# Kernel optimization log

Hardware: AMD Instinct MI355X
Metric: run time of the kernel (lower is better)

Reference implementation:

```python
import jax, jax.numpy as jnp
import numpy as np

N_NODES = 100000
N_EDGES = 1250000
IN_DIM = 128
HID_DIM = 64
OUT_DIM = 16


def setup_inputs() -> dict:
    key = jax.random.key(0)
    k1, k2, k3, k4, k5, k6, k7 = jax.random.split(key, 7)
    x = jax.random.normal(k1, (N_NODES, IN_DIM), dtype=jnp.float32)
    edge_index = jax.random.randint(k2, (2, N_EDGES), 0, N_NODES, dtype=jnp.int64)
    s = 1.0 / np.sqrt(IN_DIM)
    W1 = jax.random.uniform(k3, (IN_DIM, HID_DIM), jnp.float32, -s, s)
    b1 = jax.random.uniform(k4, (HID_DIM,), jnp.float32, -s, s)
    s2 = 1.0 / np.sqrt(HID_DIM)
    W2 = jax.random.uniform(k5, (HID_DIM, OUT_DIM), jnp.float32, -s2, s2)
    b2 = jax.random.uniform(k6, (OUT_DIM,), jnp.float32, -s2, s2)
    return {"x": x, "edge_index": edge_index, "W1": W1, "b1": b1, "W2": W2, "b2": b2}


def reference(x, edge_index, W1, b1, W2, b2):
    # GCNConv (PyG default): linear transform, add self-loops, symmetric norm,
    # gather-scatter aggregation, bias. Then relu -> linear -> log_softmax.
    N = x.shape[0]
    loop = jnp.arange(N, dtype=edge_index.dtype)
    src = jnp.concatenate([edge_index[0], loop])  # message sources
    dst = jnpp_concat = jnp.concatenate([edge_index[1], loop])  # message targets
    # degree (with self-loops) computed on destination nodes
    deg = jax.ops.segment_sum(jnp.ones_like(dst, dtype=x.dtype), dst, num_segments=N)
    deg_inv_sqrt = jnp.where(deg > 0, jax.lax.rsqrt(deg), 0.0)
    norm = deg_inv_sqrt[src] * deg_inv_sqrt[dst]  # [E+N]
    h = x @ W1  # [N, hid] -- transform before aggregation (fewer bytes moved)
    msg = h[src] * norm[:, None]  # gather: [E+N, hid]
    agg = jax.ops.segment_sum(msg, dst, num_segments=N) + b1  # scatter-add
    h = jax.nn.relu(agg)
    logits = h @ W2 + b2
    return jax.nn.log_softmax(logits, axis=-1)
```

## Files before the change

kernel.cpp:

```cpp
#include <hip/hip_runtime.h>

#define N_NODES 100000
#define N_EDGES 1250000
#define IN_DIM  128
#define HID     64
#define OUTD    16
#define ROW     64
#define NRANGE  8
#define RSIZE   12500
#define NCHUNK  128
#define CHUNK   9768
#define FILLB   (NRANGE * NCHUNK)

typedef __attribute__((ext_vector_type(8))) short  short8;
typedef __attribute__((ext_vector_type(4))) float  floatx4;

__device__ __forceinline__ unsigned short f2bf(float f) {
    unsigned u = __float_as_uint(f);
    u += 0x7fffu + ((u >> 16) & 1u);
    return (unsigned short)(u >> 16);
}
__device__ __forceinline__ float bf2f_lo(unsigned u) { return __uint_as_float(u << 16); }
__device__ __forceinline__ float bf2f_hi(unsigned u) { return __uint_as_float(u & 0xffff0000u); }

__global__ __launch_bounds__(256) void zero_cursor(int* __restrict__ cursor,
                                                   unsigned* __restrict__ hb_dummy) {
    int i = blockIdx.x * 256 + threadIdx.x;
    if (i < N_NODES) cursor[i] = 0;
    if (i < 32) hb_dummy[i] = 0u;
}

__global__ __launch_bounds__(256) void fill_kernel(const int* __restrict__ src,
                                                   const int* __restrict__ dst,
                                                   int* __restrict__ cursor,
                                                   int* __restrict__ csr) {
    const int r  = blockIdx.x & 7;
    const int c  = blockIdx.x >> 3;
    const int lo = r * RSIZE;
    const int q1 = min(N_EDGES, (c + 1) * CHUNK) >> 2;
    for (int q = (c * CHUNK >> 2) + threadIdx.x; q < q1; q += 256) {
        int4 d4 = ((const int4*)dst)[q];
        int  e  = q << 2;
#pragma unroll
        for (int u = 0; u < 4; u++) {
            int d = (u == 0) ? d4.x : (u == 1) ? d4.y : (u == 2) ? d4.z : d4.w;
            if ((unsigned)(d - lo) < (unsigned)RSIZE) {
                int s = src[e + u];
                int p = atomicAdd(&cursor[d], 1);
                if (p < ROW) csr[(size_t)d * ROW + p] = s;
            }
        }
    }
}

__global__ __launch_bounds__(256) void gemm_mfma(const float* __restrict__ x,
                                                 const float* __restrict__ W1,
                                                 const int* __restrict__ cursor,
                                                 float* __restrict__ dis,
                                                 unsigned short* __restrict__ hb) {
    __shared__ unsigned short xs[16][132];
    __shared__ unsigned short w1t[64][132];

    const int m0 = blockIdx.x * 16;

    for (int idx = threadIdx.x; idx < 16 * IN_DIM; idx += 256) {
        int m = idx >> 7, k = idx & 127;
        xs[m][k] = f2bf(x[(size_t)(m0 + m) * IN_DIM + k]);
    }
    for (int idx = threadIdx.x; idx < IN_DIM * HID; idx += 256) {
        int k = idx >> 6, n = idx & 63;
        w1t[n][k] = f2bf(W1[idx]);
    }
    __syncthreads();

    const int lane = threadIdx.x & 63;
    const int n0   = (threadIdx.x >> 6) * 16;
    const int mrow = lane & 15;
    const int quad = lane >> 4;

    floatx4 acc = {0.f, 0.f, 0.f, 0.f};
#pragma unroll
    for (int k0 = 0; k0 < IN_DIM; k0 += 32) {
        short8 a = *(const short8*)&xs[mrow][k0 + quad * 8];
        short8 b = *(const short8*)&w1t[n0 + mrow][k0 + quad * 8];
        acc = __builtin_amdgcn_mfma_f32_16x16x32_bf16(a, b, acc, 0, 0, 0);
    }

#pragma unroll
    for (int reg = 0; reg < 4; reg++) {
        int m = quad * 4 + reg;
        float di = rsqrtf((float)cursor[m0 + m] + 1.0f);
        hb[(size_t)(m0 + m) * HID + n0 + mrow] = f2bf(acc[reg] * di);
    }
    if (threadIdx.x < 16)
        dis[m0 + threadIdx.x] = rsqrtf((float)cursor[m0 + threadIdx.x] + 1.0f);
}

__global__ __launch_bounds__(256) void pull_epilogue(const unsigned short* __restrict__ hb,
                                                     const int* __restrict__ csr,
                                                     const int* __restrict__ deg,
                                                     const float* __restrict__ dis,
                                                     const float* __restrict__ b1,
                                                     const float* __restrict__ W2,
                                                     const float* __restrict__ b2,
                                                     float* __restrict__ out) {
    const int i     = blockIdx.x * 4 + (threadIdx.x >> 6);
    const int lane  = threadIdx.x & 63;
    const int e_sub = lane >> 4;
    const int f4    = lane & 15;

    const int   cnt = min(deg[i], ROW);
    const float di  = dis[i];

    int s_l = N_NODES;
    if (lane < cnt) s_l = csr[(size_t)i * ROW + lane];

    uint2 hs = ((const uint2*)(hb + (size_t)i * HID))[f4];

    float ax = 0.f, ay = 0.f, az = 0.f, aw = 0.f;
    const int G = (cnt + 3) >> 2;
    int g = 0;
    for (; g + 2 <= G; g += 2) {
        int e0 = (g << 2) + e_sub, e1 = e0 + 4;
        int s0 = __shfl(s_l, e0, 64), s1 = __shfl(s_l, e1, 64);
        uint2 a = ((const uint2*)(hb + (size_t)s0 * HID))[f4];
        uint2 b = ((const uint2*)(hb + (size_t)s1 * HID))[f4];
        ax += bf2f_lo(a.x); ay += bf2f_hi(a.x); az += bf2f_lo(a.y); aw += bf2f_hi(a.y);
        ax += bf2f_lo(b.x); ay += bf2f_hi(b.x); az += bf2f_lo(b.y); aw += bf2f_hi(b.y);
    }
    if (g < G) {
        int e0 = (g << 2) + e_sub;
        int s0 = __shfl(s_l, e0, 64);
        uint2 a = ((const uint2*)(hb + (size_t)s0 * HID))[f4];
        ax += bf2f_lo(a.x); ay += bf2f_hi(a.x); az += bf2f_lo(a.y); aw += bf2f_hi(a.y);
    }

    ax += __shfl_xor(ax, 16, 64); ax += __shfl_xor(ax, 32, 64);
    ay += __shfl_xor(ay, 16, 64); ay += __shfl_xor(ay, 32, 64);
    az += __shfl_xor(az, 16, 64); az += __shfl_xor(az, 32, 64);
    aw += __shfl_xor(aw, 16, 64); aw += __shfl_xor(aw, 32, 64);

    float4 b1v = ((const float4*)b1)[f4];
    float v0 = fmaxf(fmaf(ax + bf2f_lo(hs.x), di, b1v.x), 0.f);
    float v1 = fmaxf(fmaf(ay + bf2f_hi(hs.x), di, b1v.y), 0.f);
    float v2 = fmaxf(fmaf(az + bf2f_lo(hs.y), di, b1v.z), 0.f);
    float v3 = fmaxf(fmaf(aw + bf2f_hi(hs.y), di, b1v.w), 0.f);

    const float4* W2v = (const float4*)W2;
    float4 w0 = W2v[(4 * f4 + 0) * 4 + e_sub];
    float4 w1 = W2v[(4 * f4 + 1) * 4 + e_sub];
    float4 w2 = W2v[(4 * f4 + 2) * 4 + e_sub];
    float4 w3 = W2v[(4 * f4 + 3) * 4 + e_sub];
    float p0 = v0 * w0.x + v1 * w1.x + v2 * w2.x + v3 * w3.x;
    float p1 = v0 * w0.y + v1 * w1.y + v2 * w2.y + v3 * w3.y;
    float p2 = v0 * w0.z + v1 * w1.z + v2 * w2.z + v3 * w3.z;
    float p3 = v0 * w0.w + v1 * w1.w + v2 * w2.w + v3 * w3.w;
#pragma unroll
    for (int d = 1; d < 16; d <<= 1) {
        p0 += __shfl_xor(p0, d, 64);
        p1 += __shfl_xor(p1, d, 64);
        p2 += __shfl_xor(p2, d, 64);
        p3 += __shfl_xor(p3, d, 64);
    }
    float4 b2v = ((const float4*)b2)[e_sub];
    float lg0 = p0 + b2v.x, lg1 = p1 + b2v.y, lg2 = p2 + b2v.z, lg3 = p3 + b2v.w;

    float m = fmaxf(fmaxf(lg0, lg1), fmaxf(lg2, lg3));
    m = fmaxf(m, __shfl_xor(m, 16, 64));
    m = fmaxf(m, __shfl_xor(m, 32, 64));
    float s = __expf(lg0 - m) + __expf(lg1 - m) + __expf(lg2 - m) + __expf(lg3 - m);
    s += __shfl_xor(s, 16, 64);
    s += __shfl_xor(s, 32, 64);
    float lse = __logf(s) + m;

    if (f4 == 0) {
        float4 o = make_float4(lg0 - lse, lg1 - lse, lg2 - lse, lg3 - lse);
        ((float4*)out)[(size_t)i * 4 + e_sub] = o;
    }
}

extern "C" void kernel_launch(void* const* d_in, const int* in_sizes, int n_in,
                              void* d_out, int out_size, void* d_ws, size_t ws_size,
                              hipStream_t stream) {
    const float* x   = (const float*)d_in[0];
    const int*   ei  = (const int*)d_in[1];
    const float* W1  = (const float*)d_in[2];
    const float* b1  = (const float*)d_in[3];
    const float* W2  = (const float*)d_in[4];
    const float* b2  = (const float*)d_in[5];
    float*       out = (float*)d_out;

    const int* src = ei;
    const int* dst = ei + N_EDGES;

    char* ws = (char*)d_ws;
    size_t off = 0;
    unsigned short* hb = (unsigned short*)(ws + off);
    off += (size_t)(N_NODES + 1) * HID * 2;
    int*   csr    = (int*)  (ws + off); off += ((size_t)N_NODES * ROW + ROW) * 4;
    int*   cursor = (int*)  (ws + off); off += (size_t)N_NODES * 4;
    float* dis    = (float*)(ws + off); off += (size_t)N_NODES * 4;

    zero_cursor<<<(N_NODES + 255) / 256, 256, 0, stream>>>(
        cursor, (unsigned*)(hb + (size_t)N_NODES * HID));
    fill_kernel<<<FILLB, 256, 0, stream>>>(src, dst, cursor, csr);
    gemm_mfma<<<N_NODES / 16, 256, 0, stream>>>(x, W1, cursor, dis, hb);
    pull_epilogue<<<N_NODES / 4, 256, 0, stream>>>(hb, csr, cursor, dis, b1, W2, b2, out);
}
```

Baseline: 238.5 us.

## Compute degrees separately and fuse CSR fill with GEMM in one launch

```diff
diff --git a/kernel.cpp b/kernel.cpp
--- a/kernel.cpp
+++ b/kernel.cpp
@@ -1,4 +1,5 @@
 #include <hip/hip_runtime.h>
+#include <hip/hip_bf16.h>
 
 #define N_NODES 100000
 #define N_EDGES 1250000
@@ -11,6 +12,9 @@
 #define NCHUNK  128
 #define CHUNK   9768
 #define FILLB   (NRANGE * NCHUNK)
+#define MTILE   128
+#define GEMMB   ((N_NODES + MTILE - 1) / MTILE)
+#define DEGB    ((N_EDGES / 4 + 255) / 256)
 
 typedef __attribute__((ext_vector_type(8))) short  short8;
 typedef __attribute__((ext_vector_type(4))) float  floatx4;
@@ -20,83 +24,125 @@
     u += 0x7fffu + ((u >> 16) & 1u);
     return (unsigned short)(u >> 16);
 }
-__device__ __forceinline__ float bf2f_lo(unsigned u) { return __uint_as_float(u << 16); }
-__device__ __forceinline__ float bf2f_hi(unsigned u) { return __uint_as_float(u & 0xffff0000u); }
-
-__global__ __launch_bounds__(256) void zero_cursor(int* __restrict__ cursor,
-                                                   unsigned* __restrict__ hb_dummy) {
-    int i = blockIdx.x * 256 + threadIdx.x;
-    if (i < N_NODES) cursor[i] = 0;
-    if (i < 32) hb_dummy[i] = 0u;
-}
-
-__global__ __launch_bounds__(256) void fill_kernel(const int* __restrict__ src,
-                                                   const int* __restrict__ dst,
-                                                   int* __restrict__ cursor,
-                                                   int* __restrict__ csr) {
-    const int r  = blockIdx.x & 7;
-    const int c  = blockIdx.x >> 3;
-    const int lo = r * RSIZE;
-    const int q1 = min(N_EDGES, (c + 1) * CHUNK) >> 2;
-    for (int q = (c * CHUNK >> 2) + threadIdx.x; q < q1; q += 256) {
+__device__ __forceinline__ unsigned pk2(float lo, float hi) {
+    __hip_bfloat162 t = __float22bfloat162_rn(make_float2(lo, hi));
+    return *reinterpret_cast<unsigned*>(&t);
+}
+
+__global__ __launch_bounds__(256) void deg_hist(const int* __restrict__ dst,
+                                                int* __restrict__ deg,
+                                                float* __restrict__ hdummy) {
+    int q = blockIdx.x * 256 + threadIdx.x;
+    if (q < N_EDGES / 4) {
         int4 d4 = ((const int4*)dst)[q];
-        int  e  = q << 2;
-#pragma unroll
-        for (int u = 0; u < 4; u++) {
-            int d = (u == 0) ? d4.x : (u == 1) ? d4.y : (u == 2) ? d4.z : d4.w;
-            if ((unsigned)(d - lo) < (unsigned)RSIZE) {
-                int s = src[e + u];
-                int p = atomicAdd(&cursor[d], 1);
-                if (p < ROW) csr[(size_t)d * ROW + p] = s;
+        atomicAdd(&deg[d4.x], 1);
+        atomicAdd(&deg[d4.y], 1);
+        atomicAdd(&deg[d4.z], 1);
+        atomicAdd(&deg[d4.w], 1);
+    }
+    if (blockIdx.x == 0 && threadIdx.x < HID)
+        hdummy[threadIdx.x] = 0.f;
+}
+
+__global__ __launch_bounds__(256) void fill_gemm(const float* __restrict__ x,
+                                                 const float* __restrict__ W1,
+                                                 const int* __restrict__ src,
+                                                 const int* __restrict__ dst,
+                                                 const int* __restrict__ deg,
+                                                 int* __restrict__ cursor,
+                                                 int* __restrict__ csr,
+                                                 float* __restrict__ h,
+                                                 float* __restrict__ dis) {
+    __shared__ unsigned short w1t[HID][132];
+
+    if (blockIdx.x < FILLB) {
+        const int r  = blockIdx.x & 7;
+        const int c  = blockIdx.x >> 3;
+        const int lo = r * RSIZE;
+        const int q1 = min(N_EDGES, (c + 1) * CHUNK) >> 2;
+        for (int q = (c * CHUNK >> 2) + threadIdx.x; q < q1; q += 256) {
+            int4 d4 = ((const int4*)dst)[q];
+            int  e  = q << 2;
+#pragma unroll
+            for (int u = 0; u < 4; u++) {
+                int d = (u == 0) ? d4.x : (u == 1) ? d4.y : (u == 2) ? d4.z : d4.w;
+                if ((unsigned)(d - lo) < (unsigned)RSIZE) {
+                    int s = src[e + u];
+                    int p = atomicAdd(&cursor[d], 1);
+                    if (p < ROW) csr[(size_t)d * ROW + p] = s;
+                }
             }
         }
-    }
-}
-
-__global__ __launch_bounds__(256) void gemm_mfma(const float* __restrict__ x,
-                                                 const float* __restrict__ W1,
-                                                 const int* __restrict__ cursor,
-                                                 float* __restrict__ dis,
-                                                 unsigned short* __restrict__ hb) {
-    __shared__ unsigned short xs[16][132];
-    __shared__ unsigned short w1t[64][132];
-
-    const int m0 = blockIdx.x * 16;
-
-    for (int idx = threadIdx.x; idx < 16 * IN_DIM; idx += 256) {
-        int m = idx >> 7, k = idx & 127;
-        xs[m][k] = f2bf(x[(size_t)(m0 + m) * IN_DIM + k]);
-    }
-    for (int idx = threadIdx.x; idx < IN_DIM * HID; idx += 256) {
-        int k = idx >> 6, n = idx & 63;
-        w1t[n][k] = f2bf(W1[idx]);
+        return;
+    }
+
+    const int m0 = (blockIdx.x - FILLB) * MTILE;
+
+    for (int q = threadIdx.x; q < IN_DIM * HID / 4; q += 256) {
+        int k = q >> 4, n = (q & 15) * 4;
+        float4 wq = ((const float4*)W1)[q];
+        w1t[n + 0][k] = f2bf(wq.x);
+        w1t[n + 1][k] = f2bf(wq.y);
+        w1t[n + 2][k] = f2bf(wq.z);
+        w1t[n + 3][k] = f2bf(wq.w);
     }
     __syncthreads();
 
     const int lane = threadIdx.x & 63;
-    const int n0   = (threadIdx.x >> 6) * 16;
+    const int w    = threadIdx.x >> 6;
     const int mrow = lane & 15;
     const int quad = lane >> 4;
-
-    floatx4 acc = {0.f, 0.f, 0.f, 0.f};
+    const int rowa = min(m0 + w * 32 + mrow,      N_NODES - 1);
+    const int rowb = min(m0 + w * 32 + 16 + mrow, N_NODES - 1);
+
+    floatx4 acc[2][4] = {};
 #pragma unroll
     for (int k0 = 0; k0 < IN_DIM; k0 += 32) {
-        short8 a = *(const short8*)&xs[mrow][k0 + quad * 8];
-        short8 b = *(const short8*)&w1t[n0 + mrow][k0 + quad * 8];
-        acc = __builtin_amdgcn_mfma_f32_16x16x32_bf16(a, b, acc, 0, 0, 0);
-    }
-
-#pragma unroll
-    for (int reg = 0; reg < 4; reg++) {
-        int m = quad * 4 + reg;
-        float di = rsqrtf((float)cursor[m0 + m] + 1.0f);
-        hb[(size_t)(m0 + m) * HID + n0 + mrow] = f2bf(acc[reg] * di);
-    }
-    if (threadIdx.x < 16)
-        dis[m0 + threadIdx.x] = rsqrtf((float)cursor[m0 + threadIdx.x] + 1.0f);
-}
-
-__global__ __launch_bounds__(256) void pull_epilogue(const unsigned short* __restrict__ hb,
+        union { unsigned u[4]; short8 s; } a0, a1;
+        {
+            const float4* pa = (const float4*)(x + (size_t)rowa * IN_DIM + k0 + quad * 8);
+            float4 u0 = pa[0], v0 = pa[1];
+            a0.u[0] = pk2(u0.x, u0.y); a0.u[1] = pk2(u0.z, u0.w);
+            a0.u[2] = pk2(v0.x, v0.y); a0.u[3] = pk2(v0.z, v0.w);
+            const float4* pb = (const float4*)(x + (size_t)rowb * IN_DIM + k0 + quad * 8);
+            float4 u1 = pb[0], v1 = pb[1];
+            a1.u[0] = pk2(u1.x, u1.y); a1.u[1] = pk2(u1.z, u1.w);
+            a1.u[2] = pk2(v1.x, v1.y); a1.u[3] = pk2(v1.z, v1.w);
+        }
+        short8 b0 = *(const short8*)&w1t[ 0 + mrow][k0 + quad * 8];
+        short8 b1 = *(const short8*)&w1t[16 + mrow][k0 + quad * 8];
+        short8 b2 = *(const short8*)&w1t[32 + mrow][k0 + quad * 8];
+        short8 b3 = *(const short8*)&w1t[48 + mrow][k0 + quad * 8];
+        acc[0][0] = __builtin_amdgcn_mfma_f32_16x16x32_bf16(a0.s, b0, acc[0][0], 0, 0, 0);
+        acc[0][1] = __builtin_amdgcn_mfma_f32_16x16x32_bf16(a0.s, b1, acc[0][1], 0, 0, 0);
+        acc[0][2] = __builtin_amdgcn_mfma_f32_16x16x32_bf16(a0.s, b2, acc[0][2], 0, 0, 0);
+        acc[0][3] = __builtin_amdgcn_mfma_f32_16x16x32_bf16(a0.s, b3, acc[0][3], 0, 0, 0);
+        acc[1][0] = __builtin_amdgcn_mfma_f32_16x16x32_bf16(a1.s, b0, acc[1][0], 0, 0, 0);
+        acc[1][1] = __builtin_amdgcn_mfma_f32_16x16x32_bf16(a1.s, b1, acc[1][1], 0, 0, 0);
+        acc[1][2] = __builtin_amdgcn_mfma_f32_16x16x32_bf16(a1.s, b2, acc[1][2], 0, 0, 0);
+        acc[1][3] = __builtin_amdgcn_mfma_f32_16x16x32_bf16(a1.s, b3, acc[1][3], 0, 0, 0);
+    }
+
+#pragma unroll
+    for (int tm = 0; tm < 2; tm++) {
+#pragma unroll
+        for (int reg = 0; reg < 4; reg++) {
+            int m = m0 + w * 32 + tm * 16 + quad * 4 + reg;
+            if (m < N_NODES) {
+                float di = rsqrtf((float)deg[m] + 1.0f);
+#pragma unroll
+                for (int tn = 0; tn < 4; tn++)
+                    h[(size_t)m * HID + tn * 16 + mrow] = acc[tm][tn][reg] * di;
+            }
+        }
+    }
+    if (threadIdx.x < MTILE) {
+        int m = m0 + threadIdx.x;
+        if (m < N_NODES) dis[m] = rsqrtf((float)deg[m] + 1.0f);
+    }
+}
+
+__global__ __launch_bounds__(256) void pull_epilogue(const float* __restrict__ h,
                                                      const int* __restrict__ csr,
                                                      const int* __restrict__ deg,
                                                      const float* __restrict__ dis,
@@ -115,7 +161,7 @@
     int s_l = N_NODES;
     if (lane < cnt) s_l = csr[(size_t)i * ROW + lane];
 
-    uint2 hs = ((const uint2*)(hb + (size_t)i * HID))[f4];
+    float4 hs = ((const float4*)(h + (size_t)i * HID))[f4];
 
     float ax = 0.f, ay = 0.f, az = 0.f, aw = 0.f;
     const int G = (cnt + 3) >> 2;
@@ -123,16 +169,15 @@
     for (; g + 2 <= G; g += 2) {
         int e0 = (g << 2) + e_sub, e1 = e0 + 4;
         int s0 = __shfl(s_l, e0, 64), s1 = __shfl(s_l, e1, 64);
-        uint2 a = ((const uint2*)(hb + (size_t)s0 * HID))[f4];
-        uint2 b = ((const uint2*)(hb + (size_t)s1 * HID))[f4];
-        ax += bf2f_lo(a.x); ay += bf2f_hi(a.x); az += bf2f_lo(a.y); aw += bf2f_hi(a.y);
-        ax += bf2f_lo(b.x); ay += bf2f_hi(b.x); az += bf2f_lo(b.y); aw += bf2f_hi(b.y);
+        float4 a = ((const float4*)(h + (size_t)s0 * HID))[f4];
+        float4 b = ((const float4*)(h + (size_t)s1 * HID))[f4];
+        ax += a.x + b.x; ay += a.y + b.y; az += a.z + b.z; aw += a.w + b.w;
     }
     if (g < G) {
         int e0 = (g << 2) + e_sub;
         int s0 = __shfl(s_l, e0, 64);
-        uint2 a = ((const uint2*)(hb + (size_t)s0 * HID))[f4];
-        ax += bf2f_lo(a.x); ay += bf2f_hi(a.x); az += bf2f_lo(a.y); aw += bf2f_hi(a.y);
+        float4 a = ((const float4*)(h + (size_t)s0 * HID))[f4];
+        ax += a.x; ay += a.y; az += a.z; aw += a.w;
     }
 
     ax += __shfl_xor(ax, 16, 64); ax += __shfl_xor(ax, 32, 64);
@@ -141,10 +186,10 @@
     aw += __shfl_xor(aw, 16, 64); aw += __shfl_xor(aw, 32, 64);
 
     float4 b1v = ((const float4*)b1)[f4];
-    float v0 = fmaxf(fmaf(ax + bf2f_lo(hs.x), di, b1v.x), 0.f);
-    float v1 = fmaxf(fmaf(ay + bf2f_hi(hs.x), di, b1v.y), 0.f);
-    float v2 = fmaxf(fmaf(az + bf2f_lo(hs.y), di, b1v.z), 0.f);
-    float v3 = fmaxf(fmaf(aw + bf2f_hi(hs.y), di, b1v.w), 0.f);
+    float v0 = fmaxf(fmaf(ax + hs.x, di, b1v.x), 0.f);
+    float v1 = fmaxf(fmaf(ay + hs.y, di, b1v.y), 0.f);
+    float v2 = fmaxf(fmaf(az + hs.z, di, b1v.z), 0.f);
+    float v3 = fmaxf(fmaf(aw + hs.w, di, b1v.w), 0.f);
 
     const float4* W2v = (const float4*)W2;
     float4 w0 = W2v[(4 * f4 + 0) * 4 + e_sub];
@@ -195,15 +240,14 @@
 
     char* ws = (char*)d_ws;
     size_t off = 0;
-    unsigned short* hb = (unsigned short*)(ws + off);
-    off += (size_t)(N_NODES + 1) * HID * 2;
+    float* h      = (float*)(ws + off); off += (size_t)(N_NODES + 1) * HID * 4;
     int*   csr    = (int*)  (ws + off); off += ((size_t)N_NODES * ROW + ROW) * 4;
+    int*   deg    = (int*)  (ws + off); off += (size_t)N_NODES * 4;
     int*   cursor = (int*)  (ws + off); off += (size_t)N_NODES * 4;
     float* dis    = (float*)(ws + off); off += (size_t)N_NODES * 4;
 
-    zero_cursor<<<(N_NODES + 255) / 256, 256, 0, stream>>>(
-        cursor, (unsigned*)(hb + (size_t)N_NODES * HID));
-    fill_kernel<<<FILLB, 256, 0, stream>>>(src, dst, cursor, csr);
-    gemm_mfma<<<N_NODES / 16, 256, 0, stream>>>(x, W1, cursor, dis, hb);
-    pull_epilogue<<<N_NODES / 4, 256, 0, stream>>>(hb, csr, cursor, dis, b1, W2, b2, out);
-}
+    hipMemsetAsync(deg, 0, (size_t)2 * N_NODES * 4, stream);
+    deg_hist<<<DEGB, 256, 0, stream>>>(dst, deg, h + (size_t)N_NODES * HID);
+    fill_gemm<<<FILLB + GEMMB, 256, 0, stream>>>(x, W1, src, dst, deg, cursor, csr, h, dis);
+    pull_epilogue<<<N_NODES / 4, 256, 0, stream>>>(h, csr, deg, dis, b1, W2, b2, out);
+}
```

Result: slower. 288.4 us (+20.9%).
